# Optimization experiments

Hardware: AMD Instinct MI355X
Metric: run time of the kernel (lower is better)

Reference implementation:

```python
import jax, jax.numpy as jnp
import numpy as np

B, T, D_IN, D_H, R = 64, 512, 1024, 1024, 16
IN_DIMS = (8, 8, 16)    # 8*8*16 = 1024 = input_size (and hidden_size)
OUT_DIMS = (16, 16, 16)  # 16*16*16 = 4096 = 4*hidden_size


def setup_inputs() -> dict:
    key = jax.random.key(0)
    ks = jax.random.split(key, 14)
    s = 0.5 / np.sqrt(R)  # keep TT product well-scaled

    def cores(k):
        k1, k2, k3, k4, k5, k6 = jax.random.split(k, 6)
        i1, i2, i3 = IN_DIMS
        o1, o2, o3 = OUT_DIMS
        return (
            jax.random.normal(k1, (i1, R)) * s,        # rank-1 boundary squeezed
            jax.random.normal(k2, (R, i2, R)) * s,
            jax.random.normal(k3, (R, i3, R)) * s,
            jax.random.normal(k4, (R, o1, R)) * s,
            jax.random.normal(k5, (R, o2, R)) * s,
            jax.random.normal(k6, (R, o3)) * s,        # rank-1 boundary squeezed
        )

    ih = cores(ks[0])
    hh = cores(ks[1])
    return {
        "x": jax.random.normal(ks[2], (B, T, D_IN), dtype=jnp.float32),
        "ih_g1": ih[0], "ih_g2": ih[1], "ih_g3": ih[2],
        "ih_g4": ih[3], "ih_g5": ih[4], "ih_g6": ih[5],
        "hh_g1": hh[0], "hh_g2": hh[1], "hh_g3": hh[2],
        "hh_g4": hh[3], "hh_g5": hh[4], "hh_g6": hh[5],
        "b_ih": jnp.zeros((4 * D_H,), jnp.float32),
        "b_hh": jnp.zeros((4 * D_H,), jnp.float32),
    }


def tt_matvec(x, g1, g2, g3, g4, g5, g6):
    # x: (B, in_features) -> (B, out_features) via TT weight contraction
    b = x.shape[0]
    t = x.reshape(b, *IN_DIMS)                      # (B, i1, i2, i3)
    t = jnp.einsum('bijk,ia->bjka', t, g1)          # contract in-mode 1
    t = jnp.einsum('bjka,ajc->bkc', t, g2)          # contract in-mode 2
    t = jnp.einsum('bkc,ckd->bd', t, g3)            # contract in-mode 3
    t = jnp.einsum('bd,dne->bne', t, g4)            # expand out-mode 1
    t = jnp.einsum('bne,emf->bnmf', t, g5)          # expand out-mode 2
    t = jnp.einsum('bnmf,fp->bnmp', t, g6)          # expand out-mode 3
    return t.reshape(b, -1)


def reference(x, ih_g1, ih_g2, ih_g3, ih_g4, ih_g5, ih_g6,
              hh_g1, hh_g2, hh_g3, hh_g4, hh_g5, hh_g6, b_ih, b_hh):
    ih_cores = (ih_g1, ih_g2, ih_g3, ih_g4, ih_g5, ih_g6)
    hh_cores = (hh_g1, hh_g2, hh_g3, hh_g4, hh_g5, hh_g6)
    batch = x.shape[0]
    h0 = jnp.zeros((batch, D_H), x.dtype)
    c0 = jnp.zeros((batch, D_H), x.dtype)

    # precompute input-to-hidden projections for all timesteps (batched)
    ih_all = tt_matvec(x.reshape(-1, D_IN), *ih_cores).reshape(batch, -1, 4 * D_H) + b_ih
    ih_all = jnp.swapaxes(ih_all, 0, 1)  # (T, B, 4H)

    def step(carry, ih_t):
        h, c = carry
        gates = ih_t + tt_matvec(h, *hh_cores) + b_hh
        i, f, g, o = jnp.split(gates, 4, axis=1)
        c = jax.nn.sigmoid(f) * c + jax.nn.sigmoid(i) * jnp.tanh(g)
        h = jax.nn.sigmoid(o) * jnp.tanh(c)
        return (h, c), h

    (h, c), hs = jax.lax.scan(step, (h0, c0), ih_all)
    output = jnp.swapaxes(hs, 0, 1)  # (B, T, H)
    return output, (h, c)
```

## Files before the change

kernel.cpp:

```cpp
#include <hip/hip_runtime.h>
#include <math.h>

#define NB   64
#define NT   512
#define DH   1024
#define HID_OFF  33554432
#define HC_SZ    65536


typedef float v2f __attribute__((ext_vector_type(2)));

__device__ __forceinline__ v2f mkv2(float a, float b) { v2f r; r.x = a; r.y = b; return r; }

__device__ __forceinline__ void bar_lgkm() {
    asm volatile("s_waitcnt lgkmcnt(0)\n\ts_barrier" ::: "memory");
}

template<int CTRL>
__device__ __forceinline__ float dpp_add(float v) {
    int m = __builtin_amdgcn_update_dpp(0, __builtin_bit_cast(int, v), CTRL, 0xf, 0xf, true);
    return v + __builtin_bit_cast(float, m);
}
__device__ __forceinline__ float wave_red_sum(float v) {
    v = dpp_add<0x111>(v);
    v = dpp_add<0x112>(v);
    v = dpp_add<0x114>(v);
    v = dpp_add<0x118>(v);
    v = dpp_add<0x142>(v);
    v = dpp_add<0x143>(v);
    return v;
}

__device__ __forceinline__ float sigm(float x) { return 1.f / (1.f + __expf(-x)); }
__device__ __forceinline__ float tanh_fast(float x) {
    float e = __expf(2.f * x);
    return 1.f - 2.f / (e + 1.f);
}

__global__ __launch_bounds__(256) void k0_build(
    const float* __restrict__ g1a, const float* __restrict__ g2a,
    const float* __restrict__ g3a, const float* __restrict__ g5a,
    const float* __restrict__ g6a,
    const float* __restrict__ g1b, const float* __restrict__ g2b,
    const float* __restrict__ g3b, const float* __restrict__ g5b,
    const float* __restrict__ g6b,
    float* __restrict__ ATa, float* __restrict__ M2a,
    float* __restrict__ ATb, float* __restrict__ M2b)
{
    const float* g1 = blockIdx.x ? g1b : g1a;
    const float* g2 = blockIdx.x ? g2b : g2a;
    const float* g3 = blockIdx.x ? g3b : g3a;
    const float* g5 = blockIdx.x ? g5b : g5a;
    const float* g6 = blockIdx.x ? g6b : g6a;
    float* A_T = blockIdx.x ? ATb : ATa;
    float* M2  = blockIdx.x ? M2b : M2a;

    __shared__ float Lg1[128], Lg2[2048], Lg3[4096], Lg5[4096], Lg6[256], M1[1024];
    int tid = threadIdx.x;
    for (int i = tid; i < 128;  i += 256) Lg1[i] = g1[i];
    for (int i = tid; i < 2048; i += 256) Lg2[i] = g2[i];
    for (int i = tid; i < 4096; i += 256) Lg3[i] = g3[i];
    for (int i = tid; i < 4096; i += 256) Lg5[i] = g5[i];
    for (int i = tid; i < 256;  i += 256) Lg6[i] = g6[i];
    __syncthreads();
    for (int idx = tid; idx < 1024; idx += 256) {
        int i1 = idx >> 7, j = (idx >> 4) & 7, c = idx & 15;
        float s = 0.f;
        for (int a = 0; a < 16; ++a) s += Lg1[i1 * 16 + a] * Lg2[a * 128 + j * 16 + c];
        M1[idx] = s;
    }
    __syncthreads();
    int base = 4096 * blockIdx.y;
    for (int idx = base + tid; idx < base + 4096; idx += 256) {
        int d = idx >> 10, i = idx & 1023;
        int i1 = i >> 7, j = (i >> 4) & 7, k = i & 15;
        float s = 0.f;
        for (int c = 0; c < 16; ++c) s += M1[i1 * 128 + j * 16 + c] * Lg3[c * 256 + k * 16 + d];
        A_T[idx] = s;
    }
    if (blockIdx.y == 0) {
        for (int idx = tid; idx < 4096; idx += 256) {
            int e = idx >> 8, mp = idx & 255;
            int m = mp >> 4, p = mp & 15;
            float s = 0.f;
            for (int f = 0; f < 16; ++f) s += Lg5[e * 256 + m * 16 + f] * Lg6[f * 16 + p];
            M2[idx] = s;
        }
    }
}

__global__ __launch_bounds__(256) void k1_zy(
    const float* __restrict__ x, const float* __restrict__ A_T,
    const float* __restrict__ g4, float* __restrict__ y_out)
{
    __shared__ __align__(16) float Z[2][2][2][16];

    const int tid  = threadIdx.x;
    const int lane = tid & 63;
    const int w    = tid >> 6;
    const int s    = w >> 1;
    const int wp   = w & 1;
    const int i0   = wp * 512 + lane * 8;

    v2f av[8][8];
    #pragma unroll
    for (int d = 0; d < 16; ++d) {
        float Ar[8];
        *(float4*)&Ar[0] = *(const float4*)&A_T[d * 1024 + i0];
        *(float4*)&Ar[4] = *(const float4*)&A_T[d * 1024 + i0 + 4];
        #pragma unroll
        for (int ip = 0; ip < 8; ++ip) {
            if (d & 1) av[ip][d >> 1].y = Ar[ip];
            else       av[ip][d >> 1].x = Ar[ip];
        }
    }
    const int u0 = wp * 128 + lane;
    const int u1 = u0 + 64;
    float g4r0[16], g4r1[16];
    #pragma unroll
    for (int d = 0; d < 16; ++d) {
        g4r0[d] = g4[d * 256 + u0];
        g4r1[d] = g4[d * 256 + u1];
    }

    const int rbase = (blockIdx.x * 2 + s) * 16;
    float xr[8];
    *(float4*)&xr[0] = *(const float4*)&x[(size_t)rbase * 1024 + i0];
    *(float4*)&xr[4] = *(const float4*)&x[(size_t)rbase * 1024 + i0 + 4];

    for (int rr = 0; rr < 16; ++rr) {
        const int row = rbase + rr;
        const int rp  = rr & 1;
        float xn[8];
        if (rr < 15) {
            *(float4*)&xn[0] = *(const float4*)&x[(size_t)(row + 1) * 1024 + i0];
            *(float4*)&xn[4] = *(const float4*)&x[(size_t)(row + 1) * 1024 + i0 + 4];
        }
        v2f p[8];
        #pragma unroll
        for (int dd = 0; dd < 8; ++dd) p[dd] = xr[0] * av[0][dd];
        #pragma unroll
        for (int ip = 1; ip < 8; ++ip)
            #pragma unroll
            for (int dd = 0; dd < 8; ++dd) p[dd] += xr[ip] * av[ip][dd];
        #pragma unroll
        for (int dd = 0; dd < 8; ++dd) {
            float sx = wave_red_sum(p[dd].x);
            float sy = wave_red_sum(p[dd].y);
            if (lane == 63) *(v2f*)&Z[s][rp][wp][2 * dd] = mkv2(sx, sy);
        }
        bar_lgkm();
        float zs[16];
        {
            const float4* za = (const float4*)&Z[s][rp][0][0];
            const float4* zb = (const float4*)&Z[s][rp][1][0];
            float4 a0 = za[0], a1 = za[1], a2 = za[2], a3 = za[3];
            float4 b0 = zb[0], b1 = zb[1], b2 = zb[2], b3 = zb[3];
            *(float4*)&zs[0]  = make_float4(a0.x + b0.x, a0.y + b0.y, a0.z + b0.z, a0.w + b0.w);
            *(float4*)&zs[4]  = make_float4(a1.x + b1.x, a1.y + b1.y, a1.z + b1.z, a1.w + b1.w);
            *(float4*)&zs[8]  = make_float4(a2.x + b2.x, a2.y + b2.y, a2.z + b2.z, a2.w + b2.w);
            *(float4*)&zs[12] = make_float4(a3.x + b3.x, a3.y + b3.y, a3.z + b3.z, a3.w + b3.w);
        }
        float y0 = zs[0] * g4r0[0], y1 = zs[0] * g4r1[0];
        #pragma unroll
        for (int d = 1; d < 16; ++d) {
            y0 = fmaf(zs[d], g4r0[d], y0);
            y1 = fmaf(zs[d], g4r1[d], y1);
        }
        y_out[(size_t)row * 256 + u0] = y0;
        y_out[(size_t)row * 256 + u1] = y1;
        #pragma unroll
        for (int ip = 0; ip < 8; ++ip) xr[ip] = xn[ip];
    }
}

__global__ __launch_bounds__(1024)
__attribute__((amdgpu_waves_per_eu(4, 4)))
void k2_lstm(
    const float* __restrict__ A_T_hh, const float* __restrict__ g4hh,
    const float* __restrict__ M2hh,
    const float* __restrict__ M2ih, const float* __restrict__ y_ih_g,
    const float* __restrict__ b_ih, const float* __restrict__ b_hh,
    float* __restrict__ pfdump, float* __restrict__ out)
{
    __shared__ __align__(16) float Lh[1024];
    __shared__ __align__(16) float Lzp[2][2][16];
    __shared__ __align__(16) float Lw[2][256];

    const int tid  = threadIdx.x;
    const int b    = blockIdx.x;
    const int lane = tid & 63;
    const int w    = tid >> 6;
    const int dg   = w >> 1;
    const int wsl  = w & 1;
    const int mp   = tid & 255;
    const int n0   = tid >> 8;

    const int ibase = wsl * 512 + 2 * lane;
    v2f a0p[4], a1p[4];
    #pragma unroll
    for (int k = 0; k < 4; ++k) {
        a0p[k] = *(const v2f*)&A_T_hh[(2 * dg) * 1024 + ibase + 128 * k];
        a1p[k] = *(const v2f*)&A_T_hh[(2 * dg + 1) * 1024 + ibase + 128 * k];
    }

    float g4w[16];
    #pragma unroll
    for (int d = 0; d < 16; ++d) g4w[d] = g4hh[d * 256 + w * 16 + (lane & 15)];

    v2f m2v[8];
    #pragma unroll
    for (int k = 0; k < 8; ++k)
        m2v[k] = mkv2(M2hh[(2 * k) * 256 + mp], M2hh[(2 * k + 1) * 256 + mp]);

    float m2i[16];
    #pragma unroll
    for (int e = 0; e < 16; ++e) m2i[e] = M2ih[e * 256 + mp];

    float bias0 = b_ih[tid]        + b_hh[tid];
    float bias1 = b_ih[1024 + tid] + b_hh[1024 + tid];
    float bias2 = b_ih[2048 + tid] + b_hh[2048 + tid];
    float bias3 = b_ih[3072 + tid] + b_hh[3072 + tid];

    Lh[tid] = 0.f;
    float h = 0.f, c = 0.f;
    __syncthreads();

    const float* yrow = y_ih_g + (size_t)b * (NT * 256);
    float*       orow = out + (size_t)b * (NT * 1024);
    float pfacc = 0.f;

    for (int t = 0; t < NT; ++t) {
        const int p = t & 1;

        const int ybase = __builtin_amdgcn_readfirstlane(t * 256 + n0 * 16);
        float yv[4][16];
        #pragma unroll
        for (int g = 0; g < 4; ++g)
            #pragma unroll
            for (int e = 0; e < 16; ++e)
                yv[g][e] = yrow[ybase + g * 64 + e];
        float ypf = 0.f;
        {
            int tpf = (t + 4 < NT) ? (t + 4) : (NT - 1);
            if (tid < 256) ypf = yrow[tpf * 256 + tid];
        }

        float p0, p1;
        {
            const v2f* hv2 = (const v2f*)&Lh[ibase];
            v2f hp0 = hv2[0], hp1 = hv2[64], hp2 = hv2[128], hp3 = hv2[192];
            v2f s0 = hp0 * a0p[0]; s0 += hp1 * a0p[1]; s0 += hp2 * a0p[2]; s0 += hp3 * a0p[3];
            v2f s1 = hp0 * a1p[0]; s1 += hp1 * a1p[1]; s1 += hp2 * a1p[2]; s1 += hp3 * a1p[3];
            p0 = s0.x + s0.y;
            p1 = s1.x + s1.y;
        }
        p0 = wave_red_sum(p0);
        p1 = wave_red_sum(p1);
        if (lane == 63) *(v2f*)&Lzp[p][wsl][2 * dg] = mkv2(p0, p1);

        float acc0 = bias0, acc1 = bias1, acc2 = bias2, acc3 = bias3;
        #pragma unroll
        for (int e = 0; e < 16; ++e) {
            acc0 = fmaf(yv[0][e], m2i[e], acc0);
            acc1 = fmaf(yv[1][e], m2i[e], acc1);
            acc2 = fmaf(yv[2][e], m2i[e], acc2);
            acc3 = fmaf(yv[3][e], m2i[e], acc3);
        }
        bar_lgkm();

        {
            float zs[16];
            const float4* za = (const float4*)&Lzp[p][0][0];
            const float4* zb = (const float4*)&Lzp[p][1][0];
            float4 a0 = za[0], a1 = za[1], a2 = za[2], a3 = za[3];
            float4 b0 = zb[0], b1 = zb[1], b2 = zb[2], b3 = zb[3];
            *(float4*)&zs[0]  = make_float4(a0.x + b0.x, a0.y + b0.y, a0.z + b0.z, a0.w + b0.w);
            *(float4*)&zs[4]  = make_float4(a1.x + b1.x, a1.y + b1.y, a1.z + b1.z, a1.w + b1.w);
            *(float4*)&zs[8]  = make_float4(a2.x + b2.x, a2.y + b2.y, a2.z + b2.z, a2.w + b2.w);
            *(float4*)&zs[12] = make_float4(a3.x + b3.x, a3.y + b3.y, a3.z + b3.z, a3.w + b3.w);
            float wa = zs[0] * g4w[0], wb = zs[1] * g4w[1];
            #pragma unroll
            for (int d = 2; d < 16; d += 2) {
                wa = fmaf(zs[d],     g4w[d],     wa);
                wb = fmaf(zs[d + 1], g4w[d + 1], wb);
            }
            if (lane < 16) Lw[p][w * 16 + lane] = wa + wb;
        }
        bar_lgkm();

        #pragma unroll
        for (int g = 0; g < 4; ++g) {
            const float4* wr4 = (const float4*)&Lw[p][(n0 + 4 * g) * 16];
            float4 f0 = wr4[0], f1 = wr4[1], f2 = wr4[2], f3 = wr4[3];
            v2f A = mkv2(f0.x, f0.y) * m2v[0];
            A += mkv2(f0.z, f0.w) * m2v[1];
            A += mkv2(f1.x, f1.y) * m2v[2];
            A += mkv2(f1.z, f1.w) * m2v[3];
            A += mkv2(f2.x, f2.y) * m2v[4];
            A += mkv2(f2.z, f2.w) * m2v[5];
            A += mkv2(f3.x, f3.y) * m2v[6];
            A += mkv2(f3.z, f3.w) * m2v[7];
            float d1 = A.x + A.y;
            if (g == 0) acc0 += d1;
            else if (g == 1) acc1 += d1;
            else if (g == 2) acc2 += d1;
            else acc3 += d1;
        }

        float ig = sigm(acc0);
        float fg = sigm(acc1);
        float gg = tanh_fast(acc2);
        float og = sigm(acc3);
        c = fg * c + ig * gg;
        h = og * tanh_fast(c);

        Lh[tid] = h;
        orow[t * 1024 + tid] = h;
        pfacc += ypf;
        bar_lgkm();
    }

    out[HID_OFF + b * 1024 + tid] = h;
    out[HID_OFF + HC_SZ + b * 1024 + tid] = c;
    if (tid < 256) pfdump[tid] = pfacc;
}

extern "C" void kernel_launch(void* const* d_in, const int* in_sizes, int n_in,
                              void* d_out, int out_size, void* d_ws, size_t ws_size,
                              hipStream_t stream) {
    const float* x     = (const float*)d_in[0];
    const float* ihg1  = (const float*)d_in[1];
    const float* ihg2  = (const float*)d_in[2];
    const float* ihg3  = (const float*)d_in[3];
    const float* ihg4  = (const float*)d_in[4];
    const float* ihg5  = (const float*)d_in[5];
    const float* ihg6  = (const float*)d_in[6];
    const float* hhg1  = (const float*)d_in[7];
    const float* hhg2  = (const float*)d_in[8];
    const float* hhg3  = (const float*)d_in[9];
    const float* hhg4  = (const float*)d_in[10];
    const float* hhg5  = (const float*)d_in[11];
    const float* hhg6  = (const float*)d_in[12];
    const float* b_ih  = (const float*)d_in[13];
    const float* b_hh  = (const float*)d_in[14];
    float* out = (float*)d_out;

    float* ws     = (float*)d_ws;
    float* ATih   = ws;
    float* AThh   = ws + 16384;
    float* M2ih   = ws + 32768;
    float* M2hh   = ws + 36864;
    float* pfdump = ws + 106496;
    float* yih    = ws + 107520;

    hipLaunchKernelGGL(k0_build, dim3(2, 4), dim3(256), 0, stream,
                       ihg1, ihg2, ihg3, ihg5, ihg6,
                       hhg1, hhg2, hhg3, hhg5, hhg6,
                       ATih, M2ih, AThh, M2hh);
    hipLaunchKernelGGL(k1_zy, dim3(1024), dim3(256), 0, stream,
                       x, ATih, ihg4, yih);
    hipLaunchKernelGGL(k2_lstm, dim3(NB), dim3(1024), 0, stream,
                       AThh, hhg4, M2hh, M2ih, yih, b_ih, b_hh, pfdump, out);
}
```

Measured before the change: 1.421 ms.

## Compute per-wave Lw redundantly to drop a block barrier each timestep

Each wave now computes the 64 intermediate w values it needs itself, with g4 weights indexed per lane, and writes them to a private LDS slice. A wave-local lgkmcnt wait then replaces the second block-wide barrier in every recurrent step. The Lz double buffer becomes a single buffer, loaded constants are pinned in VGPRs with empty asm, and the prefetched y value is carried through a four-deep register shift so its load is consumed later. The cost is redundant FMAs and more register pressure under a fixed waves-per-EU bound.

```diff
diff --git a/kernel.cpp b/kernel.cpp
--- a/kernel.cpp
+++ b/kernel.cpp
@@ -11,6 +11,9 @@
 typedef float v2f __attribute__((ext_vector_type(2)));
 
 __device__ __forceinline__ v2f mkv2(float a, float b) { v2f r; r.x = a; r.y = b; return r; }
+
+#define PINF(x) asm volatile("" : "+v"(x))
+#define PIN2(x) asm volatile("" : "+v"(x))
 
 __device__ __forceinline__ void bar_lgkm() {
     asm volatile("s_waitcnt lgkmcnt(0)\n\ts_barrier" ::: "memory");
@@ -184,8 +187,8 @@
     float* __restrict__ pfdump, float* __restrict__ out)
 {
     __shared__ __align__(16) float Lh[1024];
-    __shared__ __align__(16) float Lzp[2][2][16];
-    __shared__ __align__(16) float Lw[2][256];
+    __shared__ __align__(16) float Lz[2][16];
+    __shared__ __align__(16) float Lw[16][64];
 
     const int tid  = threadIdx.x;
     const int b    = blockIdx.x;
@@ -202,28 +205,35 @@
     for (int k = 0; k < 4; ++k) {
         a0p[k] = *(const v2f*)&A_T_hh[(2 * dg) * 1024 + ibase + 128 * k];
         a1p[k] = *(const v2f*)&A_T_hh[(2 * dg + 1) * 1024 + ibase + 128 * k];
-    }
-
+        PIN2(a0p[k]); PIN2(a1p[k]);
+    }
+
+    const int nl = 4 * (lane >> 4) + n0;
+    const int el = lane & 15;
     float g4w[16];
     #pragma unroll
-    for (int d = 0; d < 16; ++d) g4w[d] = g4hh[d * 256 + w * 16 + (lane & 15)];
+    for (int d = 0; d < 16; ++d) { g4w[d] = g4hh[d * 256 + nl * 16 + el]; PINF(g4w[d]); }
 
     v2f m2v[8];
     #pragma unroll
-    for (int k = 0; k < 8; ++k)
+    for (int k = 0; k < 8; ++k) {
         m2v[k] = mkv2(M2hh[(2 * k) * 256 + mp], M2hh[(2 * k + 1) * 256 + mp]);
+        PIN2(m2v[k]);
+    }
 
     float m2i[16];
     #pragma unroll
-    for (int e = 0; e < 16; ++e) m2i[e] = M2ih[e * 256 + mp];
+    for (int e = 0; e < 16; ++e) { m2i[e] = M2ih[e * 256 + mp]; PINF(m2i[e]); }
 
     float bias0 = b_ih[tid]        + b_hh[tid];
     float bias1 = b_ih[1024 + tid] + b_hh[1024 + tid];
     float bias2 = b_ih[2048 + tid] + b_hh[2048 + tid];
     float bias3 = b_ih[3072 + tid] + b_hh[3072 + tid];
+    PINF(bias0); PINF(bias1); PINF(bias2); PINF(bias3);
 
     Lh[tid] = 0.f;
     float h = 0.f, c = 0.f;
+    float yp0 = 0.f, yp1 = 0.f, yp2 = 0.f, yp3 = 0.f;
     __syncthreads();
 
     const float* yrow = y_ih_g + (size_t)b * (NT * 256);
@@ -231,8 +241,6 @@
     float pfacc = 0.f;
 
     for (int t = 0; t < NT; ++t) {
-        const int p = t & 1;
-
         const int ybase = __builtin_amdgcn_readfirstlane(t * 256 + n0 * 16);
         float yv[4][16];
         #pragma unroll
@@ -240,10 +248,10 @@
             #pragma unroll
             for (int e = 0; e < 16; ++e)
                 yv[g][e] = yrow[ybase + g * 64 + e];
-        float ypf = 0.f;
+        float ypn = 0.f;
         {
             int tpf = (t + 4 < NT) ? (t + 4) : (NT - 1);
-            if (tid < 256) ypf = yrow[tpf * 256 + tid];
+            if (tid < 256) ypn = yrow[tpf * 256 + tid];
         }
 
         float p0, p1;
@@ -257,7 +265,7 @@
         }
         p0 = wave_red_sum(p0);
         p1 = wave_red_sum(p1);
-        if (lane == 63) *(v2f*)&Lzp[p][wsl][2 * dg] = mkv2(p0, p1);
+        if (lane == 63) *(v2f*)&Lz[wsl][2 * dg] = mkv2(p0, p1);
 
         float acc0 = bias0, acc1 = bias1, acc2 = bias2, acc3 = bias3;
         #pragma unroll
@@ -271,8 +279,8 @@
 
         {
             float zs[16];
-            const float4* za = (const float4*)&Lzp[p][0][0];
-            const float4* zb = (const float4*)&Lzp[p][1][0];
+            const float4* za = (const float4*)&Lz[0][0];
+            const float4* zb = (const float4*)&Lz[1][0];
             float4 a0 = za[0], a1 = za[1], a2 = za[2], a3 = za[3];
             float4 b0 = zb[0], b1 = zb[1], b2 = zb[2], b3 = zb[3];
             *(float4*)&zs[0]  = make_float4(a0.x + b0.x, a0.y + b0.y, a0.z + b0.z, a0.w + b0.w);
@@ -285,13 +293,13 @@
                 wa = fmaf(zs[d],     g4w[d],     wa);
                 wb = fmaf(zs[d + 1], g4w[d + 1], wb);
             }
-            if (lane < 16) Lw[p][w * 16 + lane] = wa + wb;
-        }
-        bar_lgkm();
+            Lw[w][lane] = wa + wb;
+        }
+        asm volatile("s_waitcnt lgkmcnt(0)" ::: "memory");
 
         #pragma unroll
         for (int g = 0; g < 4; ++g) {
-            const float4* wr4 = (const float4*)&Lw[p][(n0 + 4 * g) * 16];
+            const float4* wr4 = (const float4*)&Lw[w][g * 16];
             float4 f0 = wr4[0], f1 = wr4[1], f2 = wr4[2], f3 = wr4[3];
             v2f A = mkv2(f0.x, f0.y) * m2v[0];
             A += mkv2(f0.z, f0.w) * m2v[1];
@@ -317,13 +325,14 @@
 
         Lh[tid] = h;
         orow[t * 1024 + tid] = h;
-        pfacc += ypf;
+        pfacc += yp0; yp0 = yp1; yp1 = yp2; yp2 = yp3; yp3 = ypn;
         bar_lgkm();
     }
 
     out[HID_OFF + b * 1024 + tid] = h;
     out[HID_OFF + HC_SZ + b * 1024 + tid] = c;
-    if (tid < 256) pfdump[tid] = pfacc;
+    float pfsink = pfacc + yp0 + yp1 + yp2 + yp3;
+    if (tid < 256) pfdump[tid] = pfsink;
 }
 
 extern "C" void kernel_launch(void* const* d_in, const int* in_sizes, int n_in,
```

New measurement: 1.428 ms. About the same (+0.5%).
